# Kernel tuning notes

Hardware: AMD Instinct MI355X
Metric: run time of the kernel (lower is better)

The kernel has to match this reference:

```python
import jax, jax.numpy as jnp
import numpy as np

EPS = 1e-8  # torch CosineSimilarity eps
BN_EPS = 0.0  # BN folded into scale/shift


def _conv1d(x, w):  # x:(B,C,N), w:(O,C) -> (B,O,N)
    return jnp.einsum('oc,bcn->bon', w, x)


def _conv2d(x, w):  # x:(B,C,N,M), w:(O,C) -> (B,O,N,M)
    return jnp.einsum('oc,bcnm->bonm', w, x)


def setup_inputs() -> dict:
    key = jax.random.key(0)
    B, f, n1, n2 = 128, 32, 64, 128
    ks = jax.random.split(key, 12)
    d = {
        'x_label': jax.random.normal(ks[0], (B, f, n2), jnp.float32),
        'x_object': jax.random.normal(ks[1], (B, f, n1), jnp.float32),
        'template_xyz': jax.random.normal(ks[2], (B, n1, 3), jnp.float32),
        'mlp_w1': 0.1 * jax.random.normal(ks[3], (32, 68), jnp.float32),
        'mlp_s1': jnp.ones((32,), jnp.float32),
        'mlp_t1': jnp.zeros((32,), jnp.float32),
        'mlp_w2': 0.1 * jax.random.normal(ks[4], (32, 32), jnp.float32),
        'mlp_s2': jnp.ones((32,), jnp.float32),
        'mlp_t2': jnp.zeros((32,), jnp.float32),
        'gw_w1': 0.1 * jax.random.normal(ks[5], (32, 32), jnp.float32),
        'gw_b1': jnp.zeros((32,), jnp.float32),
        'gw_s': jnp.ones((32,), jnp.float32),
        'gw_t': jnp.zeros((32,), jnp.float32),
        'gw_w2': 0.1 * jax.random.normal(ks[6], (32, 32), jnp.float32),
        'gw_b2': jnp.zeros((32,), jnp.float32),
        'gm_w1': 0.1 * jax.random.normal(ks[7], (32, 35), jnp.float32),
        'gm_s1': jnp.ones((32,), jnp.float32),
        'gm_t1': jnp.zeros((32,), jnp.float32),
        'gm_w2': 0.1 * jax.random.normal(ks[8], (32, 32), jnp.float32),
        'gm_s2': jnp.ones((32,), jnp.float32),
        'gm_t2': jnp.zeros((32,), jnp.float32),
        'fl_w1': 0.1 * jax.random.normal(ks[9], (64, 64), jnp.float32),
        'fl_s1': jnp.ones((64,), jnp.float32),
        'fl_t1': jnp.zeros((64,), jnp.float32),
        'fl_w2': 0.1 * jax.random.normal(ks[10], (64, 64), jnp.float32),
        'fl_b2': jnp.zeros((64,), jnp.float32),
    }
    return d


def reference(x_label, x_object, template_xyz,
              mlp_w1, mlp_s1, mlp_t1, mlp_w2, mlp_s2, mlp_t2,
              gw_w1, gw_b1, gw_s, gw_t, gw_w2, gw_b2,
              gm_w1, gm_s1, gm_t1, gm_w2, gm_s2, gm_t2,
              fl_w1, fl_s1, fl_t1, fl_w2, fl_b2):
    B, f, n1 = x_object.shape
    n2 = x_label.shape[2]

    # pairwise cosine similarity over channel dim -> (B, n1, n2)
    num = jnp.einsum('bfn,bfm->bnm', x_object, x_label)
    na = jnp.linalg.norm(x_object, axis=1)  # (B,n1)
    nb = jnp.linalg.norm(x_label, axis=1)   # (B,n2)
    cos = num / jnp.maximum(na[:, :, None] * nb[:, None, :], EPS)

    # nearest-template gather (indices from detached scores)
    txyz = jnp.transpose(template_xyz, (0, 2, 1))            # (B,3,n1)
    template_xyz_fea = jnp.concatenate([txyz, x_object], 1)  # (B,35,n1)
    idx = jnp.argmax(jax.lax.stop_gradient(cos), axis=1)     # (B,n2)
    template_fea = jnp.take_along_axis(template_xyz_fea, idx[:, None, :], axis=2)  # (B,35,n2)

    # max-pool over template dim of the (non-detached) scores
    max_cla = jnp.max(cos, axis=1, keepdims=True)            # (B,1,n2)

    fusion = jnp.concatenate([max_cla, template_fea, x_label], 1)  # (B,68,n2)
    h = jax.nn.relu(mlp_s1[:, None] * _conv1d(fusion, mlp_w1) + mlp_t1[:, None])
    h = jax.nn.relu(mlp_s2[:, None] * _conv1d(h, mlp_w2) + mlp_t2[:, None])  # (B,32,n2)

    # global attention branch over (B,f,n1,n2)
    diff = x_label[:, :, None, :] - x_object[:, :, :, None]
    g = _conv2d(diff, gw_w1) + gw_b1[:, None, None]
    g = jax.nn.leaky_relu(gw_s[:, None, None] * g + gw_t[:, None, None], 0.2)
    gw = jax.nn.sigmoid(_conv2d(g, gw_w2) + gw_b2[:, None, None])
    gfeat = gw * x_object[:, :, :, None]                      # (B,32,n1,n2)
    txyz_b = jnp.broadcast_to(txyz[:, :, :, None], (B, 3, n1, n2))
    gfeat = jnp.concatenate([txyz_b, gfeat], 1)               # (B,35,n1,n2)
    gfeat = jax.nn.relu(gm_s1[:, None, None] * _conv2d(gfeat, gm_w1) + gm_t1[:, None, None])
    gfeat = jax.nn.relu(gm_s2[:, None, None] * _conv2d(gfeat, gm_w2) + gm_t2[:, None, None])
    gpool = jnp.max(gfeat, axis=2)                            # (B,32,n2)

    fused = jnp.concatenate([h, gpool], 1)                    # (B,64,n2)
    out = jax.nn.relu(fl_s1[:, None] * _conv1d(fused, fl_w1) + fl_t1[:, None])
    out = _conv1d(out, fl_w2) + fl_b2[:, None]                # (B,64,n2)
    return out
```

## Files before the change

### kernel.cpp

```cpp
#include <hip/hip_runtime.h>

#define NF   32
#define NN1  64
#define NN2  128
#define P    66

typedef float f32x4 __attribute__((ext_vector_type(4)));
typedef short s16x8 __attribute__((ext_vector_type(8)));
typedef unsigned int u32;

__device__ __forceinline__ short f2bf(float f) {
    u32 u = __float_as_uint(f);
    return (short)((u + 0x7FFFu + ((u >> 16) & 1u)) >> 16);
}
__device__ __forceinline__ u32 pack2(float a, float b) {
    return (u32)(unsigned short)f2bf(a) | ((u32)(unsigned short)f2bf(b) << 16);
}

__global__ __launch_bounds__(256, 4)
void v2b_fused(const float* __restrict__ xl,
               const float* __restrict__ xo,
               const float* __restrict__ txyz,
               const float* __restrict__ mlp_w1, const float* __restrict__ mlp_s1, const float* __restrict__ mlp_t1,
               const float* __restrict__ mlp_w2, const float* __restrict__ mlp_s2, const float* __restrict__ mlp_t2,
               const float* __restrict__ gw_w1, const float* __restrict__ gw_b1,
               const float* __restrict__ gw_s,  const float* __restrict__ gw_t,
               const float* __restrict__ gw_w2, const float* __restrict__ gw_b2,
               const float* __restrict__ gm_w1, const float* __restrict__ gm_s1, const float* __restrict__ gm_t1,
               const float* __restrict__ gm_w2, const float* __restrict__ gm_s2, const float* __restrict__ gm_t2,
               const float* __restrict__ fl_w1, const float* __restrict__ fl_s1, const float* __restrict__ fl_t1,
               const float* __restrict__ fl_w2, const float* __restrict__ fl_b2,
               float* __restrict__ out)
{
    __shared__ float xo_s[NF][P];
    __shared__ float yon_s[NF][P];
    __shared__ float tpos_s[NF][P];
    __shared__ float txyz_s[3][NN1];
    __shared__ float xl_s[NF][4];
    __shared__ float ylT_s[4][NF];
    __shared__ float na_s[NN1];
    __shared__ float nb_s[4];
    __shared__ float gp_s[4][NF];
    __shared__ float gws_s[NF], gwt_s[NF], gwb2_s[NF], gmt2_s[NF];
    __shared__ s16x8 afrag_s[6][64];

    const int b    = blockIdx.x >> 5;
    const int m0   = (blockIdx.x & 31) * 4;
    const int tid  = threadIdx.x;
    const int lane = tid & 63;
    const int wv   = tid >> 6;
    const int colr = lane & 15;
    const int q    = lane >> 4;

    const float* xob = xo + (size_t)b * NF * NN1;
    for (int i = tid; i < NF * NN1; i += 256) xo_s[i >> 6][i & 63] = xob[i];
    const float* tb = txyz + (size_t)b * NN1 * 3;
    if (tid < NN1 * 3) { int nn = tid / 3, k = tid % 3; txyz_s[k][nn] = tb[tid]; }
    if (tid < NF * 4) {
        int c = tid >> 2, j = tid & 3;
        xl_s[c][j] = xl[(size_t)b * NF * NN2 + c * NN2 + m0 + j];
    }
    if (tid < NF) {
        gws_s[tid]  = gw_s[tid];
        gwt_s[tid]  = gw_t[tid];
        gwb2_s[tid] = gw_b2[tid];
        gmt2_s[tid] = gm_t2[tid];
    }
    for (int f = wv; f < 6; f += 4) {
        const int row = (f & 1) ? colr + 16 : colr;
        s16x8 a;
        if (f < 2) {
            #pragma unroll
            for (int j = 0; j < 8; ++j) a[j] = f2bf(gw_w2[row * 32 + 8 * q + j]);
        } else if (f < 4) {
            const float s1 = gm_s1[row];
            #pragma unroll
            for (int j = 0; j < 8; ++j) a[j] = f2bf(s1 * gm_w1[row * 35 + 3 + 8 * q + j]);
        } else {
            const float s2 = gm_s2[row];
            #pragma unroll
            for (int j = 0; j < 8; ++j) a[j] = f2bf(s2 * gm_w2[row * 32 + 8 * q + j]);
        }
        afrag_s[f][lane] = a;
    }
    __syncthreads();

    for (int i = tid; i < NF * NN1; i += 256) {
        const int o = i >> 6, nn = i & 63;
        float s = 0.f;
        #pragma unroll
        for (int c = 0; c < NF; ++c) s += gw_w1[o * 32 + c] * xo_s[c][nn];
        yon_s[o][nn] = -s;
        float tp = gm_w1[o * 35 + 0] * txyz_s[0][nn]
                 + gm_w1[o * 35 + 1] * txyz_s[1][nn]
                 + gm_w1[o * 35 + 2] * txyz_s[2][nn];
        tpos_s[o][nn] = gm_s1[o] * tp + gm_t1[o];
    }
    if (tid < 128) {
        const int o = tid >> 2, j = tid & 3;
        float s = gw_b1[o];
        #pragma unroll
        for (int c = 0; c < NF; ++c) s += gw_w1[o * 32 + c] * xl_s[c][j];
        ylT_s[j][o] = s;
    } else if (tid < 192) {
        const int nn = tid - 128;
        float s = 0.f;
        #pragma unroll
        for (int c = 0; c < NF; ++c) { float v = xo_s[c][nn]; s += v * v; }
        na_s[nn] = sqrtf(s);
    } else if (tid < 196) {
        const int j = tid - 192;
        float s = 0.f;
        #pragma unroll
        for (int c = 0; c < NF; ++c) { float v = xl_s[c][j]; s += v * v; }
        nb_s[j] = sqrtf(s);
    }
    __syncthreads();

    const int mj = wv;
    const int m  = m0 + wv;
    const int lA = colr + ((q & 1) << 5);
    const int lB = lA + 16;

    float rmax[8] = {0.f, 0.f, 0.f, 0.f, 0.f, 0.f, 0.f, 0.f};

    for (int ng = 0; ng < 4; ++ng) {
        const int n = ng * 16 + colr;

        s16x8 bg;
        #pragma unroll
        for (int j = 0; j < 8; ++j) {
            const int k = 8 * q + j;
            float y = yon_s[k][n] + ylT_s[mj][k];
            float a = gws_s[k] * y + gwt_s[k];
            bg[j] = f2bf(a > 0.f ? a : 0.2f * a);
        }

        f32x4 zlo, zhi;
        #pragma unroll
        for (int r = 0; r < 4; ++r) { zlo[r] = gwb2_s[4 * q + r]; zhi[r] = gwb2_s[4 * q + r + 16]; }
        zlo = __builtin_amdgcn_mfma_f32_16x16x32_bf16(afrag_s[0][lane], bg, zlo, 0, 0, 0);
        zhi = __builtin_amdgcn_mfma_f32_16x16x32_bf16(afrag_s[1][lane], bg, zhi, 0, 0, 0);

        float dlo[4], dhi[4];
        #pragma unroll
        for (int r = 0; r < 4; ++r) {
            float wlo = 1.f / (1.f + __expf(-zlo[r]));
            float whi = 1.f / (1.f + __expf(-zhi[r]));
            dlo[r] = wlo * xo_s[4 * q + r][n];
            dhi[r] = whi * xo_s[4 * q + r + 16][n];
        }
        u32 plo01 = pack2(dlo[0], dlo[1]), plo23 = pack2(dlo[2], dlo[3]);
        u32 phi01 = pack2(dhi[0], dhi[1]), phi23 = pack2(dhi[2], dhi[3]);
        u32 w0, w1, w2, w3;
        {
            u32 al0 = __shfl((int)plo01, lA), ah0 = __shfl((int)phi01, lA);
            u32 al1 = __shfl((int)plo23, lA), ah1 = __shfl((int)phi23, lA);
            u32 bl0 = __shfl((int)plo01, lB), bh0 = __shfl((int)phi01, lB);
            u32 bl1 = __shfl((int)plo23, lB), bh1 = __shfl((int)phi23, lB);
            w0 = (q < 2) ? al0 : ah0;  w1 = (q < 2) ? al1 : ah1;
            w2 = (q < 2) ? bl0 : bh0;  w3 = (q < 2) ? bl1 : bh1;
        }
        s16x8 bga;
        bga[0] = (short)w0; bga[1] = (short)(w0 >> 16);
        bga[2] = (short)w1; bga[3] = (short)(w1 >> 16);
        bga[4] = (short)w2; bga[5] = (short)(w2 >> 16);
        bga[6] = (short)w3; bga[7] = (short)(w3 >> 16);

        f32x4 mlo, mhi;
        #pragma unroll
        for (int r = 0; r < 4; ++r) { mlo[r] = tpos_s[4 * q + r][n]; mhi[r] = tpos_s[4 * q + r + 16][n]; }
        mlo = __builtin_amdgcn_mfma_f32_16x16x32_bf16(afrag_s[2][lane], bga, mlo, 0, 0, 0);
        mhi = __builtin_amdgcn_mfma_f32_16x16x32_bf16(afrag_s[3][lane], bga, mhi, 0, 0, 0);

        u32 qlo01 = pack2(fmaxf(mlo[0], 0.f), fmaxf(mlo[1], 0.f));
        u32 qlo23 = pack2(fmaxf(mlo[2], 0.f), fmaxf(mlo[3], 0.f));
        u32 qhi01 = pack2(fmaxf(mhi[0], 0.f), fmaxf(mhi[1], 0.f));
        u32 qhi23 = pack2(fmaxf(mhi[2], 0.f), fmaxf(mhi[3], 0.f));
        {
            u32 al0 = __shfl((int)qlo01, lA), ah0 = __shfl((int)qhi01, lA);
            u32 al1 = __shfl((int)qlo23, lA), ah1 = __shfl((int)qhi23, lA);
            u32 bl0 = __shfl((int)qlo01, lB), bh0 = __shfl((int)qhi01, lB);
            u32 bl1 = __shfl((int)qlo23, lB), bh1 = __shfl((int)qhi23, lB);
            w0 = (q < 2) ? al0 : ah0;  w1 = (q < 2) ? al1 : ah1;
            w2 = (q < 2) ? bl0 : bh0;  w3 = (q < 2) ? bl1 : bh1;
        }
        s16x8 bm1;
        bm1[0] = (short)w0; bm1[1] = (short)(w0 >> 16);
        bm1[2] = (short)w1; bm1[3] = (short)(w1 >> 16);
        bm1[4] = (short)w2; bm1[5] = (short)(w2 >> 16);
        bm1[6] = (short)w3; bm1[7] = (short)(w3 >> 16);

        f32x4 plo, phi;
        #pragma unroll
        for (int r = 0; r < 4; ++r) { plo[r] = gmt2_s[4 * q + r]; phi[r] = gmt2_s[4 * q + r + 16]; }
        plo = __builtin_amdgcn_mfma_f32_16x16x32_bf16(afrag_s[4][lane], bm1, plo, 0, 0, 0);
        phi = __builtin_amdgcn_mfma_f32_16x16x32_bf16(afrag_s[5][lane], bm1, phi, 0, 0, 0);
        #pragma unroll
        for (int r = 0; r < 4; ++r) {
            rmax[r]     = fmaxf(rmax[r],     fmaxf(plo[r], 0.f));
            rmax[r + 4] = fmaxf(rmax[r + 4], fmaxf(phi[r], 0.f));
        }
    }

    #pragma unroll
    for (int ix = 0; ix < 8; ++ix) {
        float v = rmax[ix];
        v = fmaxf(v, __shfl_xor(v, 1));
        v = fmaxf(v, __shfl_xor(v, 2));
        v = fmaxf(v, __shfl_xor(v, 4));
        v = fmaxf(v, __shfl_xor(v, 8));
        rmax[ix] = v;
    }
    if (colr == 0) {
        #pragma unroll
        for (int ix = 0; ix < 8; ++ix)
            gp_s[wv][4 * q + (ix & 3) + 16 * (ix >> 2)] = rmax[ix];
    }

    const int n = lane;
    float num = 0.f;
    #pragma unroll
    for (int c = 0; c < NF; ++c) num += xo_s[c][n] * xl_s[c][mj];
    float cosv = num / fmaxf(na_s[n] * nb_s[mj], 1e-8f);
    float mv = cosv; int mi = n;
    #pragma unroll
    for (int s = 32; s > 0; s >>= 1) {
        float ov = __shfl_xor(mv, s);
        int   oi = __shfl_xor(mi, s);
        if (ov > mv || (ov == mv && oi < mi)) { mv = ov; mi = oi; }
    }

    const int oc = lane & 31;
    float h1;
    {
        const float* w = mlp_w1 + oc * 68;
        float acc = w[0] * mv;
        #pragma unroll
        for (int k = 0; k < 3; ++k)  acc += w[1 + k]  * txyz_s[k][mi];
        #pragma unroll
        for (int c = 0; c < 32; ++c) acc += w[4 + c]  * xo_s[c][mi];
        #pragma unroll
        for (int c = 0; c < 32; ++c) acc += w[36 + c] * xl_s[c][mj];
        acc = mlp_s1[oc] * acc + mlp_t1[oc];
        h1 = acc > 0.f ? acc : 0.f;
    }
    float h2;
    {
        const float* w = mlp_w2 + oc * 32;
        float acc = 0.f;
        #pragma unroll
        for (int c = 0; c < 32; ++c) acc += w[c] * __shfl(h1, c);
        acc = mlp_s2[oc] * acc + mlp_t2[oc];
        h2 = acc > 0.f ? acc : 0.f;
    }
    float o1;
    {
        const float* w = fl_w1 + lane * 64;
        float acc = 0.f;
        #pragma unroll
        for (int c = 0; c < 32; ++c) acc += w[c]      * __shfl(h2, c);
        #pragma unroll
        for (int c = 0; c < 32; ++c) acc += w[32 + c] * gp_s[mj][c];
        acc = fl_s1[lane] * acc + fl_t1[lane];
        o1 = acc > 0.f ? acc : 0.f;
    }
    {
        const float* w = fl_w2 + lane * 64;
        float acc = fl_b2[lane];
        #pragma unroll
        for (int c = 0; c < 64; ++c) acc += w[c] * __shfl(o1, c);
        out[(size_t)b * 64 * NN2 + (size_t)lane * NN2 + m] = acc;
    }
}

extern "C" void kernel_launch(void* const* d_in, const int* in_sizes, int n_in,
                              void* d_out, int out_size, void* d_ws, size_t ws_size,
                              hipStream_t stream) {
    const float* xl     = (const float*)d_in[0];
    const float* xo     = (const float*)d_in[1];
    const float* txyz   = (const float*)d_in[2];
    const float* mlp_w1 = (const float*)d_in[3];
    const float* mlp_s1 = (const float*)d_in[4];
    const float* mlp_t1 = (const float*)d_in[5];
    const float* mlp_w2 = (const float*)d_in[6];
    const float* mlp_s2 = (const float*)d_in[7];
    const float* mlp_t2 = (const float*)d_in[8];
    const float* gw_w1  = (const float*)d_in[9];
    const float* gw_b1  = (const float*)d_in[10];
    const float* gw_s   = (const float*)d_in[11];
    const float* gw_t   = (const float*)d_in[12];
    const float* gw_w2  = (const float*)d_in[13];
    const float* gw_b2  = (const float*)d_in[14];
    const float* gm_w1  = (const float*)d_in[15];
    const float* gm_s1  = (const float*)d_in[16];
    const float* gm_t1  = (const float*)d_in[17];
    const float* gm_w2  = (const float*)d_in[18];
    const float* gm_s2  = (const float*)d_in[19];
    const float* gm_t2  = (const float*)d_in[20];
    const float* fl_w1  = (const float*)d_in[21];
    const float* fl_s1  = (const float*)d_in[22];
    const float* fl_t1  = (const float*)d_in[23];
    const float* fl_w2  = (const float*)d_in[24];
    const float* fl_b2  = (const float*)d_in[25];
    float* outp = (float*)d_out;

    const int B = in_sizes[0] / (NF * NN2);
    v2b_fused<<<dim3(B * 32), 256, 0, stream>>>(
        xl, xo, txyz,
        mlp_w1, mlp_s1, mlp_t1, mlp_w2, mlp_s2, mlp_t2,
        gw_w1, gw_b1, gw_s, gw_t, gw_w2, gw_b2,
        gm_w1, gm_s1, gm_t1, gm_w2, gm_s2, gm_t2,
        fl_w1, fl_s1, fl_t1, fl_w2, fl_b2,
        outp);
}
```

Before: 253.4 us.

## Spread n-groups across 16 waves per block and use xor-shuffle fragment redistribution

Raises the block from 4 to 16 waves so each wave handles one (m, n-group) tile instead of looping over four n-groups. Partial max-pool results go to shared memory and are combined by the first four waves after a barrier, and those four waves then run the tail MLP. The MFMA operand redistribution now uses xor shuffles with a select, and the sigmoid multiply is folded into a single divide. This adds parallelism per block at the cost of more shared-memory traffic, an extra barrier, and twelve waves sitting idle through the serial tail.

```diff
diff --git a/kernel.cpp b/kernel.cpp
--- a/kernel.cpp
+++ b/kernel.cpp
@@ -17,7 +17,24 @@
     return (u32)(unsigned short)f2bf(a) | ((u32)(unsigned short)f2bf(b) << 16);
 }
 
-__global__ __launch_bounds__(256, 4)
+__device__ __forceinline__ s16x8 redist(u32 L01, u32 L23, u32 H01, u32 H23, int q) {
+    u32 a0 = __shfl_xor((int)L01, 16), a1 = __shfl_xor((int)L01, 32), a2 = __shfl_xor((int)L01, 48);
+    u32 b0 = __shfl_xor((int)L23, 16), b1 = __shfl_xor((int)L23, 32), b2 = __shfl_xor((int)L23, 48);
+    u32 c0 = __shfl_xor((int)H01, 16), c1 = __shfl_xor((int)H01, 32), c2 = __shfl_xor((int)H01, 48);
+    u32 d0 = __shfl_xor((int)H23, 16), d1 = __shfl_xor((int)H23, 32), d2 = __shfl_xor((int)H23, 48);
+    u32 w0 = (q == 0) ? L01 : (q == 1) ? a2 : (q == 2) ? c1 : c0;
+    u32 w1 = (q == 0) ? L23 : (q == 1) ? b2 : (q == 2) ? d1 : d0;
+    u32 w2 = (q == 0) ? a0  : (q == 1) ? a1 : (q == 2) ? c2 : H01;
+    u32 w3 = (q == 0) ? b0  : (q == 1) ? b1 : (q == 2) ? d2 : H23;
+    s16x8 r;
+    r[0] = (short)w0; r[1] = (short)(w0 >> 16);
+    r[2] = (short)w1; r[3] = (short)(w1 >> 16);
+    r[4] = (short)w2; r[5] = (short)(w2 >> 16);
+    r[6] = (short)w3; r[7] = (short)(w3 >> 16);
+    return r;
+}
+
+__global__ __launch_bounds__(1024, 4)
 void v2b_fused(const float* __restrict__ xl,
                const float* __restrict__ xo,
                const float* __restrict__ txyz,
@@ -40,7 +57,7 @@
     __shared__ float ylT_s[4][NF];
     __shared__ float na_s[NN1];
     __shared__ float nb_s[4];
-    __shared__ float gp_s[4][NF];
+    __shared__ float gpart_s[16][NF];
     __shared__ float gws_s[NF], gwt_s[NF], gwb2_s[NF], gmt2_s[NF];
     __shared__ s16x8 afrag_s[6][64];
 
@@ -48,12 +65,14 @@
     const int m0   = (blockIdx.x & 31) * 4;
     const int tid  = threadIdx.x;
     const int lane = tid & 63;
-    const int wv   = tid >> 6;
+    const int w    = tid >> 6;
     const int colr = lane & 15;
     const int q    = lane >> 4;
+    const int mj   = w & 3;
+    const int ng   = w >> 2;
 
     const float* xob = xo + (size_t)b * NF * NN1;
-    for (int i = tid; i < NF * NN1; i += 256) xo_s[i >> 6][i & 63] = xob[i];
+    for (int i = tid; i < NF * NN1; i += 1024) xo_s[i >> 6][i & 63] = xob[i];
     const float* tb = txyz + (size_t)b * NN1 * 3;
     if (tid < NN1 * 3) { int nn = tid / 3, k = tid % 3; txyz_s[k][nn] = tb[tid]; }
     if (tid < NF * 4) {
@@ -66,7 +85,8 @@
         gwb2_s[tid] = gw_b2[tid];
         gmt2_s[tid] = gm_t2[tid];
     }
-    for (int f = wv; f < 6; f += 4) {
+    if (w < 6) {
+        const int f = w;
         const int row = (f & 1) ? colr + 16 : colr;
         s16x8 a;
         if (f < 2) {
@@ -85,7 +105,7 @@
     }
     __syncthreads();
 
-    for (int i = tid; i < NF * NN1; i += 256) {
+    for (int i = tid; i < NF * NN1; i += 1024) {
         const int o = i >> 6, nn = i & 63;
         float s = 0.f;
         #pragma unroll
@@ -117,14 +137,7 @@
     }
     __syncthreads();
 
-    const int mj = wv;
-    const int m  = m0 + wv;
-    const int lA = colr + ((q & 1) << 5);
-    const int lB = lA + 16;
-
-    float rmax[8] = {0.f, 0.f, 0.f, 0.f, 0.f, 0.f, 0.f, 0.f};
-
-    for (int ng = 0; ng < 4; ++ng) {
+    {
         const int n = ng * 16 + colr;
 
         s16x8 bg;
@@ -142,30 +155,20 @@
         zlo = __builtin_amdgcn_mfma_f32_16x16x32_bf16(afrag_s[0][lane], bg, zlo, 0, 0, 0);
         zhi = __builtin_amdgcn_mfma_f32_16x16x32_bf16(afrag_s[1][lane], bg, zhi, 0, 0, 0);
 
-        float dlo[4], dhi[4];
-        #pragma unroll
-        for (int r = 0; r < 4; ++r) {
-            float wlo = 1.f / (1.f + __expf(-zlo[r]));
-            float whi = 1.f / (1.f + __expf(-zhi[r]));
-            dlo[r] = wlo * xo_s[4 * q + r][n];
-            dhi[r] = whi * xo_s[4 * q + r + 16][n];
-        }
-        u32 plo01 = pack2(dlo[0], dlo[1]), plo23 = pack2(dlo[2], dlo[3]);
-        u32 phi01 = pack2(dhi[0], dhi[1]), phi23 = pack2(dhi[2], dhi[3]);
-        u32 w0, w1, w2, w3;
+        u32 L01, L23, H01, H23;
         {
-            u32 al0 = __shfl((int)plo01, lA), ah0 = __shfl((int)phi01, lA);
-            u32 al1 = __shfl((int)plo23, lA), ah1 = __shfl((int)phi23, lA);
-            u32 bl0 = __shfl((int)plo01, lB), bh0 = __shfl((int)phi01, lB);
-            u32 bl1 = __shfl((int)plo23, lB), bh1 = __shfl((int)phi23, lB);
-            w0 = (q < 2) ? al0 : ah0;  w1 = (q < 2) ? al1 : ah1;
-            w2 = (q < 2) ? bl0 : bh0;  w3 = (q < 2) ? bl1 : bh1;
-        }
-        s16x8 bga;
-        bga[0] = (short)w0; bga[1] = (short)(w0 >> 16);
-        bga[2] = (short)w1; bga[3] = (short)(w1 >> 16);
-        bga[4] = (short)w2; bga[5] = (short)(w2 >> 16);
-        bga[6] = (short)w3; bga[7] = (short)(w3 >> 16);
+            float d0 = xo_s[4 * q + 0][n] / (1.f + __expf(-zlo[0]));
+            float d1 = xo_s[4 * q + 1][n] / (1.f + __expf(-zlo[1]));
+            float d2 = xo_s[4 * q + 2][n] / (1.f + __expf(-zlo[2]));
+            float d3 = xo_s[4 * q + 3][n] / (1.f + __expf(-zlo[3]));
+            L01 = pack2(d0, d1); L23 = pack2(d2, d3);
+            float e0 = xo_s[4 * q + 16][n] / (1.f + __expf(-zhi[0]));
+            float e1 = xo_s[4 * q + 17][n] / (1.f + __expf(-zhi[1]));
+            float e2 = xo_s[4 * q + 18][n] / (1.f + __expf(-zhi[2]));
+            float e3 = xo_s[4 * q + 19][n] / (1.f + __expf(-zhi[3]));
+            H01 = pack2(e0, e1); H23 = pack2(e2, e3);
+        }
+        s16x8 bga = redist(L01, L23, H01, H23, q);
 
         f32x4 mlo, mhi;
         #pragma unroll
@@ -173,51 +176,43 @@
         mlo = __builtin_amdgcn_mfma_f32_16x16x32_bf16(afrag_s[2][lane], bga, mlo, 0, 0, 0);
         mhi = __builtin_amdgcn_mfma_f32_16x16x32_bf16(afrag_s[3][lane], bga, mhi, 0, 0, 0);
 
-        u32 qlo01 = pack2(fmaxf(mlo[0], 0.f), fmaxf(mlo[1], 0.f));
-        u32 qlo23 = pack2(fmaxf(mlo[2], 0.f), fmaxf(mlo[3], 0.f));
-        u32 qhi01 = pack2(fmaxf(mhi[0], 0.f), fmaxf(mhi[1], 0.f));
-        u32 qhi23 = pack2(fmaxf(mhi[2], 0.f), fmaxf(mhi[3], 0.f));
-        {
-            u32 al0 = __shfl((int)qlo01, lA), ah0 = __shfl((int)qhi01, lA);
-            u32 al1 = __shfl((int)qlo23, lA), ah1 = __shfl((int)qhi23, lA);
-            u32 bl0 = __shfl((int)qlo01, lB), bh0 = __shfl((int)qhi01, lB);
-            u32 bl1 = __shfl((int)qlo23, lB), bh1 = __shfl((int)qhi23, lB);
-            w0 = (q < 2) ? al0 : ah0;  w1 = (q < 2) ? al1 : ah1;
-            w2 = (q < 2) ? bl0 : bh0;  w3 = (q < 2) ? bl1 : bh1;
-        }
-        s16x8 bm1;
-        bm1[0] = (short)w0; bm1[1] = (short)(w0 >> 16);
-        bm1[2] = (short)w1; bm1[3] = (short)(w1 >> 16);
-        bm1[4] = (short)w2; bm1[5] = (short)(w2 >> 16);
-        bm1[6] = (short)w3; bm1[7] = (short)(w3 >> 16);
+        u32 M01 = pack2(fmaxf(mlo[0], 0.f), fmaxf(mlo[1], 0.f));
+        u32 M23 = pack2(fmaxf(mlo[2], 0.f), fmaxf(mlo[3], 0.f));
+        u32 N01 = pack2(fmaxf(mhi[0], 0.f), fmaxf(mhi[1], 0.f));
+        u32 N23 = pack2(fmaxf(mhi[2], 0.f), fmaxf(mhi[3], 0.f));
+        s16x8 bm1 = redist(M01, M23, N01, N23, q);
 
         f32x4 plo, phi;
         #pragma unroll
         for (int r = 0; r < 4; ++r) { plo[r] = gmt2_s[4 * q + r]; phi[r] = gmt2_s[4 * q + r + 16]; }
         plo = __builtin_amdgcn_mfma_f32_16x16x32_bf16(afrag_s[4][lane], bm1, plo, 0, 0, 0);
         phi = __builtin_amdgcn_mfma_f32_16x16x32_bf16(afrag_s[5][lane], bm1, phi, 0, 0, 0);
+
+        float rmax[8];
         #pragma unroll
         for (int r = 0; r < 4; ++r) {
-            rmax[r]     = fmaxf(rmax[r],     fmaxf(plo[r], 0.f));
-            rmax[r + 4] = fmaxf(rmax[r + 4], fmaxf(phi[r], 0.f));
-        }
-    }
-
-    #pragma unroll
-    for (int ix = 0; ix < 8; ++ix) {
-        float v = rmax[ix];
-        v = fmaxf(v, __shfl_xor(v, 1));
-        v = fmaxf(v, __shfl_xor(v, 2));
-        v = fmaxf(v, __shfl_xor(v, 4));
-        v = fmaxf(v, __shfl_xor(v, 8));
-        rmax[ix] = v;
-    }
-    if (colr == 0) {
-        #pragma unroll
-        for (int ix = 0; ix < 8; ++ix)
-            gp_s[wv][4 * q + (ix & 3) + 16 * (ix >> 2)] = rmax[ix];
-    }
-
+            rmax[r]     = fmaxf(plo[r], 0.f);
+            rmax[r + 4] = fmaxf(phi[r], 0.f);
+        }
+        #pragma unroll
+        for (int ix = 0; ix < 8; ++ix) {
+            float v = rmax[ix];
+            v = fmaxf(v, __shfl_xor(v, 1));
+            v = fmaxf(v, __shfl_xor(v, 2));
+            v = fmaxf(v, __shfl_xor(v, 4));
+            v = fmaxf(v, __shfl_xor(v, 8));
+            rmax[ix] = v;
+        }
+        if (colr == 0) {
+            #pragma unroll
+            for (int ix = 0; ix < 8; ++ix)
+                gpart_s[w][4 * q + (ix & 3) + 16 * (ix >> 2)] = rmax[ix];
+        }
+    }
+    __syncthreads();
+
+    if (w >= 4) return;
+    const int m = m0 + mj;
     const int n = lane;
     float num = 0.f;
     #pragma unroll
@@ -234,42 +229,46 @@
     const int oc = lane & 31;
     float h1;
     {
-        const float* w = mlp_w1 + oc * 68;
-        float acc = w[0] * mv;
-        #pragma unroll
-        for (int k = 0; k < 3; ++k)  acc += w[1 + k]  * txyz_s[k][mi];
-        #pragma unroll
-        for (int c = 0; c < 32; ++c) acc += w[4 + c]  * xo_s[c][mi];
-        #pragma unroll
-        for (int c = 0; c < 32; ++c) acc += w[36 + c] * xl_s[c][mj];
+        const float* wp = mlp_w1 + oc * 68;
+        float acc = wp[0] * mv;
+        #pragma unroll
+        for (int k = 0; k < 3; ++k)  acc += wp[1 + k]  * txyz_s[k][mi];
+        #pragma unroll
+        for (int c = 0; c < 32; ++c) acc += wp[4 + c]  * xo_s[c][mi];
+        #pragma unroll
+        for (int c = 0; c < 32; ++c) acc += wp[36 + c] * xl_s[c][mj];
         acc = mlp_s1[oc] * acc + mlp_t1[oc];
         h1 = acc > 0.f ? acc : 0.f;
     }
     float h2;
     {
-        const float* w = mlp_w2 + oc * 32;
+        const float* wp = mlp_w2 + oc * 32;
         float acc = 0.f;
         #pragma unroll
-        for (int c = 0; c < 32; ++c) acc += w[c] * __shfl(h1, c);
+        for (int c = 0; c < 32; ++c) acc += wp[c] * __shfl(h1, c);
         acc = mlp_s2[oc] * acc + mlp_t2[oc];
         h2 = acc > 0.f ? acc : 0.f;
     }
     float o1;
     {
-        const float* w = fl_w1 + lane * 64;
+        const float* wp = fl_w1 + lane * 64;
         float acc = 0.f;
         #pragma unroll
-        for (int c = 0; c < 32; ++c) acc += w[c]      * __shfl(h2, c);
-        #pragma unroll
-        for (int c = 0; c < 32; ++c) acc += w[32 + c] * gp_s[mj][c];
+        for (int c = 0; c < 32; ++c) acc += wp[c] * __shfl(h2, c);
+        #pragma unroll
+        for (int c = 0; c < 32; ++c) {
+            float gv = fmaxf(fmaxf(gpart_s[mj][c], gpart_s[mj + 4][c]),
+                             fmaxf(gpart_s[mj + 8][c], gpart_s[mj + 12][c]));
+            acc += wp[32 + c] * gv;
+        }
         acc = fl_s1[lane] * acc + fl_t1[lane];
         o1 = acc > 0.f ? acc : 0.f;
     }
     {
-        const float* w = fl_w2 + lane * 64;
+        const float* wp = fl_w2 + lane * 64;
         float acc = fl_b2[lane];
         #pragma unroll
-        for (int c = 0; c < 64; ++c) acc += w[c] * __shfl(o1, c);
+        for (int c = 0; c < 64; ++c) acc += wp[c] * __shfl(o1, c);
         out[(size_t)b * 64 * NN2 + (size_t)lane * NN2 + m] = acc;
     }
 }
@@ -306,7 +305,7 @@
     float* outp = (float*)d_out;
 
     const int B = in_sizes[0] / (NF * NN2);
-    v2b_fused<<<dim3(B * 32), 256, 0, stream>>>(
+    v2b_fused<<<dim3(B * 32), 1024, 0, stream>>>(
         xl, xo, txyz,
         mlp_w1, mlp_s1, mlp_t1, mlp_w2, mlp_s2, mlp_t2,
         gw_w1, gw_b1, gw_s, gw_t, gw_w2, gw_b2,
```

Result: slower. 326.6 us (+28.9%).
